# Kernel tuning notes

Measured on AMD Instinct MI355X. Metric: run time of the kernel, lower is better.

The kernel has to match this reference:

```python
import jax, jax.numpy as jnp
import numpy as np

B, C, N = 2, 64, 40000
MLP = [64, 64, 128]
EPS = 1e-5


def setup_inputs() -> dict:
    key = jax.random.key(0)
    ks = jax.random.split(key, 2 + 4 * len(MLP))
    inp = {
        "points": jax.random.normal(ks[0], (B, C, N), dtype=jnp.float32),
        "near_idx": jax.random.randint(ks[1], (N, 6), 0, 2 * N, dtype=jnp.int32),
    }
    last = 2 * C
    for i, out_ch in enumerate(MLP):
        k = 2 + 4 * i
        scale = 1.0 / np.sqrt(last)
        inp[f"W{i}"] = jax.random.normal(ks[k], (out_ch, last), dtype=jnp.float32) * scale
        inp[f"b{i}"] = jax.random.normal(ks[k + 1], (out_ch,), dtype=jnp.float32) * 0.01
        inp[f"g{i}"] = jnp.ones((out_ch,), dtype=jnp.float32)
        inp[f"beta{i}"] = jnp.zeros((out_ch,), dtype=jnp.float32)
        last = out_ch
    return inp


def _mlp_bn_relu(x, W, b, g, beta):
    # x: [B, N, 6, Cin]; 1x1 conv == channel matmul
    y = jnp.einsum("bnkc,oc->bnko", x, W) + b
    mu = y.mean(axis=(0, 1, 2))
    var = y.var(axis=(0, 1, 2))  # biased, matches BN training normalization
    y = (y - mu) * jax.lax.rsqrt(var + EPS) * g + beta
    return jax.nn.relu(y)


def reference(points, near_idx, W0, b0, g0, beta0, W1, b1, g1, beta1, W2, b2, g2, beta2):
    x = jnp.transpose(points, (0, 2, 1))          # [B, N, C]
    pad = jnp.full_like(x, -1.0)                  # out-of-index block (-1 fill)
    xpad = jnp.concatenate([x, pad], axis=1)      # [B, 2N, C]
    near = xpad[:, near_idx, :]                   # [B, N, 6, C] irregular gather
    feat = jnp.concatenate(
        [jnp.broadcast_to(x[:, :, None, :], near.shape), near], axis=3
    )                                             # [B, N, 6, 2C]
    feat = _mlp_bn_relu(feat, W0, b0, g0, beta0)
    feat = _mlp_bn_relu(feat, W1, b1, g1, beta1)
    feat = _mlp_bn_relu(feat, W2, b2, g2, beta2)  # [B, N, 6, C']
    new_feature = feat.max(axis=2)                # max over 6 neighbors -> [B, N, C']
    new_feature = jnp.transpose(new_feature, (0, 2, 1))  # [B, C', N] (torch layout)
    out_feature = new_feature.max(axis=1)         # max over channels -> [B, N]
    return (out_feature, new_feature)
```

## Files before the change

kernel.cpp:

```cpp
#include <hip/hip_runtime.h>

typedef unsigned short u16;
typedef unsigned int uint;
typedef short bf16x8 __attribute__((ext_vector_type(8)));
typedef float f32x4 __attribute__((ext_vector_type(4)));

constexpr int B_ = 2;
constexpr int N_ = 40000;
constexpr int SPB = 240000;
constexpr int S_ = B_ * SPB;
constexpr float EPS_ = 1e-5f;
constexpr float INV_S = 1.0f / (float)S_;
constexpr int OF_ = B_ * N_;

constexpr int WS_V_U16    = B_ * N_ * 128;
constexpr int WS_STATS_F  = WS_V_U16 / 2;
constexpr int WS_NEG2_F   = WS_STATS_F + 512;
constexpr int WS_PACK_U16 = WS_V_U16 + 2 * (512 + 64);
constexpr int MP_OFF  = 0;
constexpr int W1P_OFF = 8192;
constexpr int W2P_OFF = 12288;

__device__ inline float b2f_lo(uint u) { return __builtin_bit_cast(float, u << 16); }
__device__ inline float b2f_hi(uint u) { return __builtin_bit_cast(float, u & 0xffff0000u); }
__device__ inline float b2fu(u16 s)    { return __builtin_bit_cast(float, ((uint)s) << 16); }
__device__ inline u16 f2b(float f) {
    uint b = __builtin_bit_cast(uint, f);
    return (u16)((b + 0x7fffu + ((b >> 16) & 1u)) >> 16);
}
__device__ inline void unp8(uint4 q, float* f) {
    f[0] = b2f_lo(q.x); f[1] = b2f_hi(q.x); f[2] = b2f_lo(q.y); f[3] = b2f_hi(q.y);
    f[4] = b2f_lo(q.z); f[5] = b2f_hi(q.z); f[6] = b2f_lo(q.w); f[7] = b2f_hi(q.w);
}
__device__ inline uint fmap(float f) {
    int i = __float_as_int(f);
    return (i >= 0) ? ((uint)i | 0x80000000u) : ~(uint)i;
}
__device__ inline float funmap(uint u) {
    int i = (u & 0x80000000u) ? (int)(u & 0x7fffffffu) : (int)~u;
    return __int_as_float(i);
}

__global__ __launch_bounds__(256) void wprep_kernel(const float* __restrict__ W0,
                                                    const float* __restrict__ W1,
                                                    const float* __restrict__ W2,
                                                    float* __restrict__ stats,
                                                    float* __restrict__ neg2,
                                                    u16* __restrict__ pack) {
    const int t = threadIdx.x;
    stats[t] = 0.f; stats[t + 256] = 0.f;
    if (t < 64) {
        float s = 0.f;
        for (int j = 0; j < 64; ++j) s += W0[t * 128 + 64 + j];
        neg2[t] = -s;
    }
    for (int g = t; g < 40 * 64; g += 256) {
        int lane = g & 63, grp = g >> 6;
        int cb = lane & 15, kq = lane >> 4;
        ushort4 lo, hi;
        u16* dst;
        if (grp < 16) {
            int ct = grp >> 1, kk = grp & 1;
            int c = ct * 16 + cb, jb = kk * 32 + kq * 8;
            dst = pack + MP_OFF + g * 8;
            float v[8];
            #pragma unroll
            for (int i = 0; i < 8; ++i)
                v[i] = (c < 64) ? W0[c * 128 + jb + i] : W0[(c - 64) * 128 + 64 + jb + i];
            lo = {f2b(v[0]), f2b(v[1]), f2b(v[2]), f2b(v[3])};
            hi = {f2b(v[4]), f2b(v[5]), f2b(v[6]), f2b(v[7])};
        } else if (grp < 24) {
            int g2 = grp - 16;
            int ct = g2 >> 1, kk = g2 & 1;
            const float* wp = W1 + (ct * 16 + cb) * 64 + kk * 32 + kq * 8;
            dst = pack + W1P_OFF + (g2 * 64 + lane) * 8;
            lo = {f2b(wp[0]), f2b(wp[1]), f2b(wp[2]), f2b(wp[3])};
            hi = {f2b(wp[4]), f2b(wp[5]), f2b(wp[6]), f2b(wp[7])};
        } else {
            int g3 = grp - 24;
            int ct = g3 >> 1, kk = g3 & 1;
            const float* wp = W2 + (ct * 16 + cb) * 64 + kk * 32 + kq * 8;
            dst = pack + W2P_OFF + (g3 * 64 + lane) * 8;
            lo = {f2b(wp[0]), f2b(wp[1]), f2b(wp[2]), f2b(wp[3])};
            hi = {f2b(wp[4]), f2b(wp[5]), f2b(wp[6]), f2b(wp[7])};
        }
        *(ushort4*)dst = lo;
        *(ushort4*)(dst + 4) = hi;
    }
}

__global__ __launch_bounds__(256) void p0_kernel(const float* __restrict__ pts,
                                                 const u16* __restrict__ pack,
                                                 u16* __restrict__ V) {
    const int t = threadIdx.x, lane = t & 63, w = t >> 6;
    const int cb = lane & 15, kq = lane >> 4;
    const int b = blockIdx.y;
    const int n0 = blockIdx.x * 192 + w * 48;
    const uint4* mp = (const uint4*)(pack + MP_OFF);

    bf16x8 af[3][2];
    #pragma unroll
    for (int mt = 0; mt < 3; ++mt) {
        int n = n0 + mt * 16 + cb;
        int nc = (n < N_) ? n : (N_ - 1);
        const float* xp = pts + b * 64 * N_ + nc;
        #pragma unroll
        for (int kk = 0; kk < 2; ++kk) {
            int jb = kk * 32 + kq * 8;
            #pragma unroll
            for (int i = 0; i < 8; ++i)
                af[mt][kk][i] = (short)f2b(xp[(size_t)(jb + i) * N_]);
        }
    }
    #pragma unroll
    for (int ct = 0; ct < 8; ++ct) {
        bf16x8 b0 = __builtin_bit_cast(bf16x8, mp[(ct * 2 + 0) * 64 + lane]);
        bf16x8 b1 = __builtin_bit_cast(bf16x8, mp[(ct * 2 + 1) * 64 + lane]);
        #pragma unroll
        for (int mt = 0; mt < 3; ++mt) {
            f32x4 acc = {};
            acc = __builtin_amdgcn_mfma_f32_16x16x32_bf16(af[mt][0], b0, acc, 0, 0, 0);
            acc = __builtin_amdgcn_mfma_f32_16x16x32_bf16(af[mt][1], b1, acc, 0, 0, 0);
            int rbase = n0 + mt * 16 + kq * 4;
            #pragma unroll
            for (int r = 0; r < 4; ++r) {
                int n = rbase + r;
                if (n < N_) V[(size_t)(b * N_ + n) * 128 + ct * 16 + cb] = f2b(acc[r]);
            }
        }
    }
}

__global__ __launch_bounds__(256) void p1_kernel(const u16* __restrict__ V,
                                                 const int* __restrict__ nidx,
                                                 const float* __restrict__ neg2,
                                                 float* __restrict__ stats) {
    const int t = threadIdx.x;
    const int c = t & 63, sg = t >> 6;
    const int b = blockIdx.y;
    const int n0 = blockIdx.x * 32;
    const float ng = neg2[c];
    float sum = 0.f, sq = 0.f;
    for (int i = 0; i < 8; ++i) {
        int n = n0 + sg * 8 + i;
        float v1 = b2fu(V[(size_t)(b * N_ + n) * 128 + c]);
        #pragma unroll
        for (int k = 0; k < 6; ++k) {
            int m = nidx[n * 6 + k];
            float v2 = (m < N_) ? b2fu(V[(size_t)(b * N_ + m) * 128 + 64 + c]) : ng;
            float z = v1 + v2;
            sum += z; sq += z * z;
        }
    }
    __shared__ float red[2][4][64];
    red[0][sg][c] = sum;
    red[1][sg][c] = sq;
    __syncthreads();
    if (t < 64) {
        float s0 = (red[0][0][t] + red[0][1][t]) + (red[0][2][t] + red[0][3][t]);
        float q0 = (red[1][0][t] + red[1][1][t]) + (red[1][2][t] + red[1][3][t]);
        atomicAdd(&stats[t], s0);
        atomicAdd(&stats[64 + t], q0);
    }
}

__device__ inline bf16x8 build_af(const u16* __restrict__ V, int row1, int row2,
                                  const float* adt0, const float* adt1,
                                  const float* ngs, int j0) {
    float v1f[8], v2f[8];
    uint4 q1 = *(const uint4*)(V + (size_t)row1 * 128 + j0);
    unp8(q1, v1f);
    if (row2 >= 0) {
        uint4 q2 = *(const uint4*)(V + (size_t)row2 * 128 + 64 + j0);
        unp8(q2, v2f);
    } else {
        #pragma unroll
        for (int i = 0; i < 8; ++i) v2f[i] = ngs[j0 + i];
    }
    bf16x8 r;
    #pragma unroll
    for (int i = 0; i < 8; ++i) {
        float f0 = fmaxf((v1f[i] + v2f[i]) * adt0[j0 + i] + adt1[j0 + i], 0.f);
        r[i] = (short)f2b(f0);
    }
    return r;
}

__global__ __launch_bounds__(256) void p2_kernel(const u16* __restrict__ V,
                                                 const int* __restrict__ nidx,
                                                 const float* __restrict__ neg2,
                                                 const u16* __restrict__ pack,
                                                 const float* __restrict__ g0,
                                                 const float* __restrict__ beta0,
                                                 float* __restrict__ stats) {
    __shared__ float adt0[64], adt1[64], ngs[64];
    __shared__ float red[2][4][64];
    const int t = threadIdx.x, lane = t & 63, w = t >> 6;
    const int cb = lane & 15, kq = lane >> 4;
    if (t < 64) {
        float mu = stats[t] * INV_S, vr = stats[64 + t] * INV_S - mu * mu;
        float a = rsqrtf(vr + EPS_) * g0[t];
        adt0[t] = a; adt1[t] = beta0[t] - mu * a; ngs[t] = neg2[t];
    }
    __syncthreads();
    const int b = blockIdx.y;
    const int slb = blockIdx.x * 192 + w * 48;
    const uint4* w1p = (const uint4*)(pack + W1P_OFF);

    bf16x8 bf[4][2];
    #pragma unroll
    for (int ct = 0; ct < 4; ++ct)
        #pragma unroll
        for (int kk = 0; kk < 2; ++kk)
            bf[ct][kk] = __builtin_bit_cast(bf16x8, w1p[(ct * 2 + kk) * 64 + lane]);

    f32x4 acc[3][4] = {};
    #pragma unroll
    for (int mt = 0; mt < 3; ++mt) {
        int sl = slb + mt * 16 + cb;
        int n = sl / 6;
        int m = nidx[sl];
        int row1 = b * N_ + n;
        int row2 = (m < N_) ? (b * N_ + m) : -1;
        bf16x8 af[2];
        #pragma unroll
        for (int kk = 0; kk < 2; ++kk)
            af[kk] = build_af(V, row1, row2, adt0, adt1, ngs, kk * 32 + kq * 8);
        #pragma unroll
        for (int ct = 0; ct < 4; ++ct) {
            acc[mt][ct] = __builtin_amdgcn_mfma_f32_16x16x32_bf16(af[0], bf[ct][0], acc[mt][ct], 0, 0, 0);
            acc[mt][ct] = __builtin_amdgcn_mfma_f32_16x16x32_bf16(af[1], bf[ct][1], acc[mt][ct], 0, 0, 0);
        }
    }
    float ssum[4] = {0,0,0,0}, ssq[4] = {0,0,0,0};
    #pragma unroll
    for (int mt = 0; mt < 3; ++mt)
        #pragma unroll
        for (int ct = 0; ct < 4; ++ct)
            #pragma unroll
            for (int r = 0; r < 4; ++r) {
                float z = acc[mt][ct][r];
                ssum[ct] += z; ssq[ct] += z * z;
            }
    #pragma unroll
    for (int ct = 0; ct < 4; ++ct) {
        ssum[ct] += __shfl_xor(ssum[ct], 16); ssum[ct] += __shfl_xor(ssum[ct], 32);
        ssq[ct]  += __shfl_xor(ssq[ct], 16);  ssq[ct]  += __shfl_xor(ssq[ct], 32);
    }
    if (lane < 16) {
        #pragma unroll
        for (int ct = 0; ct < 4; ++ct) {
            red[0][w][ct * 16 + lane] = ssum[ct];
            red[1][w][ct * 16 + lane] = ssq[ct];
        }
    }
    __syncthreads();
    if (t < 64) {
        float s = (red[0][0][t] + red[0][1][t]) + (red[0][2][t] + red[0][3][t]);
        float q = (red[1][0][t] + red[1][1][t]) + (red[1][2][t] + red[1][3][t]);
        atomicAdd(&stats[128 + t], s);
        atomicAdd(&stats[192 + t], q);
    }
}

__global__ __launch_bounds__(256) void p3_kernel(const u16* __restrict__ V,
                                                 const int* __restrict__ nidx,
                                                 const float* __restrict__ neg2,
                                                 const u16* __restrict__ pack,
                                                 const float* __restrict__ g0, const float* __restrict__ beta0,
                                                 const float* __restrict__ g1, const float* __restrict__ beta1,
                                                 const float* __restrict__ g2,
                                                 float* __restrict__ stats,
                                                 float* __restrict__ out) {
    __shared__ u16  f1s[4][3072];
    __shared__ uint bmax[32][128];
    __shared__ float adt0[64], adt1[64], adt2[64], adt3[64], ngs[64];
    __shared__ float psign[128];
    __shared__ float red[2][4][128];
    const int t = threadIdx.x, lane = t & 63, w = t >> 6;
    const int cb = lane & 15, kq = lane >> 4;
    if (t < 64) {
        float mu0 = stats[t] * INV_S, vr0 = stats[64 + t] * INV_S - mu0 * mu0;
        float a0 = rsqrtf(vr0 + EPS_) * g0[t];
        adt0[t] = a0; adt1[t] = beta0[t] - mu0 * a0;
        float mu1 = stats[128 + t] * INV_S, vr1 = stats[192 + t] * INV_S - mu1 * mu1;
        float a1 = rsqrtf(vr1 + EPS_) * g1[t];
        adt2[t] = a1; adt3[t] = beta1[t] - mu1 * a1;
        ngs[t] = neg2[t];
    }
    if (t < 128) psign[t] = (g2[t] >= 0.f) ? 1.f : -1.f;
    #pragma unroll
    for (int i = 0; i < 16; ++i) ((uint*)bmax)[t + 256 * i] = 0u;
    __syncthreads();

    const int b = blockIdx.y;
    const int slb = blockIdx.x * 192 + w * 48;
    const uint4* w1p = (const uint4*)(pack + W1P_OFF);
    const uint4* w2p = (const uint4*)(pack + W2P_OFF);

    bf16x8 bf1[4][2];
    #pragma unroll
    for (int ct = 0; ct < 4; ++ct)
        #pragma unroll
        for (int kk = 0; kk < 2; ++kk)
            bf1[ct][kk] = __builtin_bit_cast(bf16x8, w1p[(ct * 2 + kk) * 64 + lane]);
    f32x4 acc1[3][4] = {};
    #pragma unroll
    for (int mt = 0; mt < 3; ++mt) {
        int sl = slb + mt * 16 + cb;
        int n = sl / 6;
        int m = nidx[sl];
        int row1 = b * N_ + n;
        int row2 = (m < N_) ? (b * N_ + m) : -1;
        bf16x8 af[2];
        #pragma unroll
        for (int kk = 0; kk < 2; ++kk)
            af[kk] = build_af(V, row1, row2, adt0, adt1, ngs, kk * 32 + kq * 8);
        #pragma unroll
        for (int ct = 0; ct < 4; ++ct) {
            acc1[mt][ct] = __builtin_amdgcn_mfma_f32_16x16x32_bf16(af[0], bf1[ct][0], acc1[mt][ct], 0, 0, 0);
            acc1[mt][ct] = __builtin_amdgcn_mfma_f32_16x16x32_bf16(af[1], bf1[ct][1], acc1[mt][ct], 0, 0, 0);
        }
    }
    u16* fb = f1s[w];
    #pragma unroll
    for (int mt = 0; mt < 3; ++mt)
        #pragma unroll
        for (int ct = 0; ct < 4; ++ct) {
            float a1c = adt2[ct * 16 + cb], d1c = adt3[ct * 16 + cb];
            #pragma unroll
            for (int r = 0; r < 4; ++r) {
                float f1 = fmaxf(acc1[mt][ct][r] * a1c + d1c, 0.f);
                int rl = mt * 16 + kq * 4 + r;
                fb[rl * 64 + ((ct * 16 + cb) ^ ((rl & 7) << 3))] = f2b(f1);
            }
        }
    float ssum[8] = {0,0,0,0,0,0,0,0}, ssq[8] = {0,0,0,0,0,0,0,0};
    #pragma unroll
    for (int half = 0; half < 2; ++half) {
        bf16x8 bf2[4][2];
        #pragma unroll
        for (int ct = 0; ct < 4; ++ct)
            #pragma unroll
            for (int kk = 0; kk < 2; ++kk)
                bf2[ct][kk] = __builtin_bit_cast(bf16x8, w2p[((half * 4 + ct) * 2 + kk) * 64 + lane]);
        f32x4 acc2[3][4] = {};
        #pragma unroll
        for (int mt = 0; mt < 3; ++mt) {
            int rl = mt * 16 + cb;
            bf16x8 af2[2];
            #pragma unroll
            for (int kk = 0; kk < 2; ++kk) {
                int j0 = kk * 32 + kq * 8;
                uint4 q = *(const uint4*)(fb + rl * 64 + (j0 ^ ((rl & 7) << 3)));
                af2[kk] = __builtin_bit_cast(bf16x8, q);
            }
            #pragma unroll
            for (int ct = 0; ct < 4; ++ct) {
                acc2[mt][ct] = __builtin_amdgcn_mfma_f32_16x16x32_bf16(af2[0], bf2[ct][0], acc2[mt][ct], 0, 0, 0);
                acc2[mt][ct] = __builtin_amdgcn_mfma_f32_16x16x32_bf16(af2[1], bf2[ct][1], acc2[mt][ct], 0, 0, 0);
            }
        }
        #pragma unroll
        for (int ct = 0; ct < 4; ++ct) {
            int c2 = half * 64 + ct * 16 + cb;
            float ps = psign[c2];
            #pragma unroll
            for (int mt = 0; mt < 3; ++mt) {
                int base = mt * 16 + kq * 4;
                int nb = 6 - (base % 6); nb = (nb > 4) ? 4 : nb;
                int nl = w * 8 + base / 6;
                float m1 = -3.402823466e+38f, m2 = -3.402823466e+38f;
                #pragma unroll
                for (int r = 0; r < 4; ++r) {
                    float z = acc2[mt][ct][r];
                    ssum[half * 4 + ct] += z;
                    ssq[half * 4 + ct] += z * z;
                    float zz = z * ps;
                    m1 = (r < nb) ? fmaxf(m1, zz) : m1;
                    m2 = (r < nb) ? m2 : fmaxf(m2, zz);
                }
                atomicMax(&bmax[nl][c2], fmap(m1));
                if (nb < 4) atomicMax(&bmax[nl + 1][c2], fmap(m2));
            }
        }
    }
    #pragma unroll
    for (int j = 0; j < 8; ++j) {
        ssum[j] += __shfl_xor(ssum[j], 16); ssum[j] += __shfl_xor(ssum[j], 32);
        ssq[j]  += __shfl_xor(ssq[j], 16);  ssq[j]  += __shfl_xor(ssq[j], 32);
    }
    if (lane < 16) {
        #pragma unroll
        for (int j = 0; j < 8; ++j) {
            int c = (j >> 2) * 64 + (j & 3) * 16 + lane;
            red[0][w][c] = ssum[j];
            red[1][w][c] = ssq[j];
        }
    }
    __syncthreads();
    if (t < 128) {
        float s = (red[0][0][t] + red[0][1][t]) + (red[0][2][t] + red[0][3][t]);
        float q = (red[1][0][t] + red[1][1][t]) + (red[1][2][t] + red[1][3][t]);
        atomicAdd(&stats[256 + t], s);
        atomicAdd(&stats[384 + t], q);
    }
    {
        int c2 = t >> 1, nh = t & 1;
        float ps = psign[c2];
        float* op = out + OF_ + ((size_t)b * 128 + c2) * N_ + blockIdx.x * 32 + nh * 16;
        #pragma unroll
        for (int i4 = 0; i4 < 4; ++i4) {
            float4 v;
            v.x = funmap(bmax[nh * 16 + i4 * 4 + 0][c2]) * ps;
            v.y = funmap(bmax[nh * 16 + i4 * 4 + 1][c2]) * ps;
            v.z = funmap(bmax[nh * 16 + i4 * 4 + 2][c2]) * ps;
            v.w = funmap(bmax[nh * 16 + i4 * 4 + 3][c2]) * ps;
            *(float4*)(op + i4 * 4) = v;
        }
    }
}

__global__ __launch_bounds__(256) void p4_kernel(const float* __restrict__ g2,
                                                 const float* __restrict__ beta2,
                                                 const float* __restrict__ stats,
                                                 float* __restrict__ outbuf) {
    __shared__ float a2s[128], d2s[128];
    const int t = threadIdx.x;
    if (t < 128) {
        float mu = stats[256 + t] * INV_S;
        float vr = stats[384 + t] * INV_S - mu * mu;
        float a = rsqrtf(vr + EPS_) * g2[t];
        a2s[t] = a;
        d2s[t] = beta2[t] - mu * a;
    }
    __syncthreads();
    const int b = blockIdx.y;
    const int n = blockIdx.x * 256 + t;
    if (n >= N_) return;
    float vmax = -3.402823466e+38f;
    #pragma unroll 8
    for (int c2 = 0; c2 < 128; ++c2) {
        size_t idx = OF_ + ((size_t)b * 128 + c2) * N_ + n;
        float v = fmaxf(outbuf[idx] * a2s[c2] + d2s[c2], 0.f);
        outbuf[idx] = v;
        vmax = fmaxf(vmax, v);
    }
    outbuf[b * N_ + n] = vmax;
}

extern "C" void kernel_launch(void* const* d_in, const int* in_sizes, int n_in,
                              void* d_out, int out_size, void* d_ws, size_t ws_size,
                              hipStream_t stream) {
    (void)in_sizes; (void)n_in; (void)out_size; (void)ws_size;
    const float* pts   = (const float*)d_in[0];
    const int*   nidx  = (const int*)d_in[1];
    const float* W0    = (const float*)d_in[2];
    const float* g0    = (const float*)d_in[4];
    const float* beta0 = (const float*)d_in[5];
    const float* W1    = (const float*)d_in[6];
    const float* g1    = (const float*)d_in[8];
    const float* beta1 = (const float*)d_in[9];
    const float* W2    = (const float*)d_in[10];
    const float* g2    = (const float*)d_in[12];
    const float* beta2 = (const float*)d_in[13];
    u16*   V     = (u16*)d_ws;
    float* stats = (float*)d_ws + WS_STATS_F;
    float* neg2  = (float*)d_ws + WS_NEG2_F;
    u16*   pack  = (u16*)d_ws + WS_PACK_U16;
    float* out   = (float*)d_out;

    hipLaunchKernelGGL(wprep_kernel, dim3(1), dim3(256), 0, stream, W0, W1, W2, stats, neg2, pack);
    hipLaunchKernelGGL(p0_kernel, dim3((N_ + 191) / 192, B_), dim3(256), 0, stream, pts, pack, V);
    hipLaunchKernelGGL(p1_kernel, dim3(N_ / 32, B_), dim3(256), 0, stream, V, nidx, neg2, stats);
    hipLaunchKernelGGL(p2_kernel, dim3(SPB / 192, B_), dim3(256), 0, stream, V, nidx, neg2, pack, g0, beta0, stats);
    hipLaunchKernelGGL(p3_kernel, dim3(SPB / 192, B_), dim3(256), 0, stream, V, nidx, neg2, pack,
                       g0, beta0, g1, beta1, g2, stats, out);
    hipLaunchKernelGGL(p4_kernel, dim3((N_ + 255) / 256, B_), dim3(256), 0, stream, g2, beta2, stats, out);
}
```

Baseline: 367.8 us.

## Cache layer-0 activations in workspace and vectorize p1 stats gather

```diff
diff --git a/kernel.cpp b/kernel.cpp
--- a/kernel.cpp
+++ b/kernel.cpp
@@ -12,18 +12,13 @@
 constexpr float EPS_ = 1e-5f;
 constexpr float INV_S = 1.0f / (float)S_;
 constexpr int OF_ = B_ * N_;
-
-constexpr int WS_V_U16    = B_ * N_ * 128;
-constexpr int WS_STATS_F  = WS_V_U16 / 2;
-constexpr int WS_NEG2_F   = WS_STATS_F + 512;
-constexpr int WS_PACK_U16 = WS_V_U16 + 2 * (512 + 64);
-constexpr int MP_OFF  = 0;
-constexpr int W1P_OFF = 8192;
-constexpr int W2P_OFF = 12288;
+constexpr int TILES_PB = SPB / 48;
+
+constexpr int      WS_V_U16   = B_ * N_ * 128;
+constexpr size_t   NEED_BIG_B = 81955072ull;
 
 __device__ inline float b2f_lo(uint u) { return __builtin_bit_cast(float, u << 16); }
 __device__ inline float b2f_hi(uint u) { return __builtin_bit_cast(float, u & 0xffff0000u); }
-__device__ inline float b2fu(u16 s)    { return __builtin_bit_cast(float, ((uint)s) << 16); }
 __device__ inline u16 f2b(float f) {
     uint b = __builtin_bit_cast(uint, f);
     return (u16)((b + 0x7fffu + ((b >> 16) & 1u)) >> 16);
@@ -62,7 +57,7 @@
         if (grp < 16) {
             int ct = grp >> 1, kk = grp & 1;
             int c = ct * 16 + cb, jb = kk * 32 + kq * 8;
-            dst = pack + MP_OFF + g * 8;
+            dst = pack + g * 8;
             float v[8];
             #pragma unroll
             for (int i = 0; i < 8; ++i)
@@ -73,14 +68,14 @@
             int g2 = grp - 16;
             int ct = g2 >> 1, kk = g2 & 1;
             const float* wp = W1 + (ct * 16 + cb) * 64 + kk * 32 + kq * 8;
-            dst = pack + W1P_OFF + (g2 * 64 + lane) * 8;
+            dst = pack + 8192 + (g2 * 64 + lane) * 8;
             lo = {f2b(wp[0]), f2b(wp[1]), f2b(wp[2]), f2b(wp[3])};
             hi = {f2b(wp[4]), f2b(wp[5]), f2b(wp[6]), f2b(wp[7])};
         } else {
             int g3 = grp - 24;
             int ct = g3 >> 1, kk = g3 & 1;
             const float* wp = W2 + (ct * 16 + cb) * 64 + kk * 32 + kq * 8;
-            dst = pack + W2P_OFF + (g3 * 64 + lane) * 8;
+            dst = pack + 12288 + (g3 * 64 + lane) * 8;
             lo = {f2b(wp[0]), f2b(wp[1]), f2b(wp[2]), f2b(wp[3])};
             hi = {f2b(wp[4]), f2b(wp[5]), f2b(wp[6]), f2b(wp[7])};
         }
@@ -96,7 +91,7 @@
     const int cb = lane & 15, kq = lane >> 4;
     const int b = blockIdx.y;
     const int n0 = blockIdx.x * 192 + w * 48;
-    const uint4* mp = (const uint4*)(pack + MP_OFF);
+    const uint4* mp = (const uint4*)pack;
 
     bf16x8 af[3][2];
     #pragma unroll
@@ -135,32 +130,47 @@
                                                  const int* __restrict__ nidx,
                                                  const float* __restrict__ neg2,
                                                  float* __restrict__ stats) {
-    const int t = threadIdx.x;
-    const int c = t & 63, sg = t >> 6;
+    const int t = threadIdx.x, lane = t & 63, w = t >> 6;
+    const int slot = lane >> 3, cg = lane & 7;
     const int b = blockIdx.y;
-    const int n0 = blockIdx.x * 32;
-    const float ng = neg2[c];
-    float sum = 0.f, sq = 0.f;
+    const int s0 = blockIdx.x * 384 + w * 96;
+    float ngs8[8];
+    #pragma unroll
+    for (int i = 0; i < 8; ++i) ngs8[i] = neg2[cg * 8 + i];
+    float sum[8] = {0,0,0,0,0,0,0,0}, sq[8] = {0,0,0,0,0,0,0,0};
+    #pragma unroll 4
+    for (int it = 0; it < 12; ++it) {
+        int s = s0 + it * 8 + slot;
+        int n = s / 6;
+        int m = nidx[s];
+        bool valid = (m < N_);
+        int row2 = valid ? (b * N_ + m) : 0;
+        uint4 q1 = *(const uint4*)(V + (size_t)(b * N_ + n) * 128 + cg * 8);
+        uint4 q2 = *(const uint4*)(V + (size_t)row2 * 128 + 64 + cg * 8);
+        float v1[8], v2[8];
+        unp8(q1, v1); unp8(q2, v2);
+        #pragma unroll
+        for (int i = 0; i < 8; ++i) {
+            float z = v1[i] + (valid ? v2[i] : ngs8[i]);
+            sum[i] += z; sq[i] = fmaf(z, z, sq[i]);
+        }
+    }
+    #pragma unroll
     for (int i = 0; i < 8; ++i) {
-        int n = n0 + sg * 8 + i;
-        float v1 = b2fu(V[(size_t)(b * N_ + n) * 128 + c]);
-        #pragma unroll
-        for (int k = 0; k < 6; ++k) {
-            int m = nidx[n * 6 + k];
-            float v2 = (m < N_) ? b2fu(V[(size_t)(b * N_ + m) * 128 + 64 + c]) : ng;
-            float z = v1 + v2;
-            sum += z; sq += z * z;
-        }
+        sum[i] += __shfl_xor(sum[i], 8); sum[i] += __shfl_xor(sum[i], 16); sum[i] += __shfl_xor(sum[i], 32);
+        sq[i]  += __shfl_xor(sq[i], 8);  sq[i]  += __shfl_xor(sq[i], 16);  sq[i]  += __shfl_xor(sq[i], 32);
     }
     __shared__ float red[2][4][64];
-    red[0][sg][c] = sum;
-    red[1][sg][c] = sq;
+    if (slot == 0) {
+        #pragma unroll
+        for (int i = 0; i < 8; ++i) { red[0][w][cg * 8 + i] = sum[i]; red[1][w][cg * 8 + i] = sq[i]; }
+    }
     __syncthreads();
     if (t < 64) {
-        float s0 = (red[0][0][t] + red[0][1][t]) + (red[0][2][t] + red[0][3][t]);
-        float q0 = (red[1][0][t] + red[1][1][t]) + (red[1][2][t] + red[1][3][t]);
-        atomicAdd(&stats[t], s0);
-        atomicAdd(&stats[64 + t], q0);
+        float s_ = (red[0][0][t] + red[0][1][t]) + (red[0][2][t] + red[0][3][t]);
+        float q_ = (red[1][0][t] + red[1][1][t]) + (red[1][2][t] + red[1][3][t]);
+        atomicAdd(&stats[t], s_);
+        atomicAdd(&stats[64 + t], q_);
     }
 }
 
@@ -186,13 +196,15 @@
     return r;
 }
 
+template<int STOREF0>
 __global__ __launch_bounds__(256) void p2_kernel(const u16* __restrict__ V,
                                                  const int* __restrict__ nidx,
                                                  const float* __restrict__ neg2,
                                                  const u16* __restrict__ pack,
                                                  const float* __restrict__ g0,
                                                  const float* __restrict__ beta0,
-                                                 float* __restrict__ stats) {
+                                                 float* __restrict__ stats,
+                                                 u16* __restrict__ f0buf) {
     __shared__ float adt0[64], adt1[64], ngs[64];
     __shared__ float red[2][4][64];
     const int t = threadIdx.x, lane = t & 63, w = t >> 6;
@@ -205,7 +217,8 @@
     __syncthreads();
     const int b = blockIdx.y;
     const int slb = blockIdx.x * 192 + w * 48;
-    const uint4* w1p = (const uint4*)(pack + W1P_OFF);
+    const uint4* w1p = (const uint4*)(pack + 8192);
+    uint4* ftile = STOREF0 ? ((uint4*)f0buf + ((size_t)b * TILES_PB + blockIdx.x * 4 + w) * (6 * 64)) : nullptr;
 
     bf16x8 bf[4][2];
     #pragma unroll
@@ -224,8 +237,11 @@
         int row2 = (m < N_) ? (b * N_ + m) : -1;
         bf16x8 af[2];
         #pragma unroll
-        for (int kk = 0; kk < 2; ++kk)
+        for (int kk = 0; kk < 2; ++kk) {
             af[kk] = build_af(V, row1, row2, adt0, adt1, ngs, kk * 32 + kq * 8);
+            if constexpr (STOREF0)
+                ftile[(mt * 2 + kk) * 64 + lane] = __builtin_bit_cast(uint4, af[kk]);
+        }
         #pragma unroll
         for (int ct = 0; ct < 4; ++ct) {
             acc[mt][ct] = __builtin_amdgcn_mfma_f32_16x16x32_bf16(af[0], bf[ct][0], acc[mt][ct], 0, 0, 0);
@@ -263,6 +279,7 @@
     }
 }
 
+template<int LOADF0>
 __global__ __launch_bounds__(256) void p3_kernel(const u16* __restrict__ V,
                                                  const int* __restrict__ nidx,
                                                  const float* __restrict__ neg2,
@@ -271,6 +288,7 @@
                                                  const float* __restrict__ g1, const float* __restrict__ beta1,
                                                  const float* __restrict__ g2,
                                                  float* __restrict__ stats,
+                                                 const u16* __restrict__ f0buf,
                                                  float* __restrict__ out) {
     __shared__ u16  f1s[4][3072];
     __shared__ uint bmax[32][128];
@@ -280,13 +298,15 @@
     const int t = threadIdx.x, lane = t & 63, w = t >> 6;
     const int cb = lane & 15, kq = lane >> 4;
     if (t < 64) {
-        float mu0 = stats[t] * INV_S, vr0 = stats[64 + t] * INV_S - mu0 * mu0;
-        float a0 = rsqrtf(vr0 + EPS_) * g0[t];
-        adt0[t] = a0; adt1[t] = beta0[t] - mu0 * a0;
+        if constexpr (!LOADF0) {
+            float mu0 = stats[t] * INV_S, vr0 = stats[64 + t] * INV_S - mu0 * mu0;
+            float a0 = rsqrtf(vr0 + EPS_) * g0[t];
+            adt0[t] = a0; adt1[t] = beta0[t] - mu0 * a0;
+            ngs[t] = neg2[t];
+        }
         float mu1 = stats[128 + t] * INV_S, vr1 = stats[192 + t] * INV_S - mu1 * mu1;
         float a1 = rsqrtf(vr1 + EPS_) * g1[t];
         adt2[t] = a1; adt3[t] = beta1[t] - mu1 * a1;
-        ngs[t] = neg2[t];
     }
     if (t < 128) psign[t] = (g2[t] >= 0.f) ? 1.f : -1.f;
     #pragma unroll
@@ -295,8 +315,9 @@
 
     const int b = blockIdx.y;
     const int slb = blockIdx.x * 192 + w * 48;
-    const uint4* w1p = (const uint4*)(pack + W1P_OFF);
-    const uint4* w2p = (const uint4*)(pack + W2P_OFF);
+    const uint4* w1p = (const uint4*)(pack + 8192);
+    const uint4* w2p = (const uint4*)(pack + 12288);
+    const uint4* ftile = LOADF0 ? ((const uint4*)f0buf + ((size_t)b * TILES_PB + blockIdx.x * 4 + w) * (6 * 64)) : nullptr;
 
     bf16x8 bf1[4][2];
     #pragma unroll
@@ -307,15 +328,20 @@
     f32x4 acc1[3][4] = {};
     #pragma unroll
     for (int mt = 0; mt < 3; ++mt) {
-        int sl = slb + mt * 16 + cb;
-        int n = sl / 6;
-        int m = nidx[sl];
-        int row1 = b * N_ + n;
-        int row2 = (m < N_) ? (b * N_ + m) : -1;
         bf16x8 af[2];
-        #pragma unroll
-        for (int kk = 0; kk < 2; ++kk)
-            af[kk] = build_af(V, row1, row2, adt0, adt1, ngs, kk * 32 + kq * 8);
+        if constexpr (LOADF0) {
+            af[0] = __builtin_bit_cast(bf16x8, ftile[(mt * 2 + 0) * 64 + lane]);
+            af[1] = __builtin_bit_cast(bf16x8, ftile[(mt * 2 + 1) * 64 + lane]);
+        } else {
+            int sl = slb + mt * 16 + cb;
+            int n = sl / 6;
+            int m = nidx[sl];
+            int row1 = b * N_ + n;
+            int row2 = (m < N_) ? (b * N_ + m) : -1;
+            #pragma unroll
+            for (int kk = 0; kk < 2; ++kk)
+                af[kk] = build_af(V, row1, row2, adt0, adt1, ngs, kk * 32 + kq * 8);
+        }
         #pragma unroll
         for (int ct = 0; ct < 4; ++ct) {
             acc1[mt][ct] = __builtin_amdgcn_mfma_f32_16x16x32_bf16(af[0], bf1[ct][0], acc1[mt][ct], 0, 0, 0);
@@ -452,7 +478,7 @@
 extern "C" void kernel_launch(void* const* d_in, const int* in_sizes, int n_in,
                               void* d_out, int out_size, void* d_ws, size_t ws_size,
                               hipStream_t stream) {
-    (void)in_sizes; (void)n_in; (void)out_size; (void)ws_size;
+    (void)in_sizes; (void)n_in; (void)out_size;
     const float* pts   = (const float*)d_in[0];
     const int*   nidx  = (const int*)d_in[1];
     const float* W0    = (const float*)d_in[2];
@@ -464,17 +490,27 @@
     const float* W2    = (const float*)d_in[10];
     const float* g2    = (const float*)d_in[12];
     const float* beta2 = (const float*)d_in[13];
+    const bool big = ws_size >= NEED_BIG_B;
     u16*   V     = (u16*)d_ws;
-    float* stats = (float*)d_ws + WS_STATS_F;
-    float* neg2  = (float*)d_ws + WS_NEG2_F;
-    u16*   pack  = (u16*)d_ws + WS_PACK_U16;
+    u16*   f0b   = big ? ((u16*)d_ws + WS_V_U16) : nullptr;
+    float* stats = (float*)d_ws + (big ? 20480000 : 5120000);
+    float* neg2  = stats + 512;
+    u16*   pack  = (u16*)d_ws + (big ? 40961152 : 10241152);
     float* out   = (float*)d_out;
 
     hipLaunchKernelGGL(wprep_kernel, dim3(1), dim3(256), 0, stream, W0, W1, W2, stats, neg2, pack);
     hipLaunchKernelGGL(p0_kernel, dim3((N_ + 191) / 192, B_), dim3(256), 0, stream, pts, pack, V);
-    hipLaunchKernelGGL(p1_kernel, dim3(N_ / 32, B_), dim3(256), 0, stream, V, nidx, neg2, stats);
-    hipLaunchKernelGGL(p2_kernel, dim3(SPB / 192, B_), dim3(256), 0, stream, V, nidx, neg2, pack, g0, beta0, stats);
-    hipLaunchKernelGGL(p3_kernel, dim3(SPB / 192, B_), dim3(256), 0, stream, V, nidx, neg2, pack,
-                       g0, beta0, g1, beta1, g2, stats, out);
+    hipLaunchKernelGGL(p1_kernel, dim3(SPB / 384, B_), dim3(256), 0, stream, V, nidx, neg2, stats);
+    if (big) {
+        hipLaunchKernelGGL((p2_kernel<1>), dim3(SPB / 192, B_), dim3(256), 0, stream,
+                           V, nidx, neg2, pack, g0, beta0, stats, f0b);
+        hipLaunchKernelGGL((p3_kernel<1>), dim3(SPB / 192, B_), dim3(256), 0, stream,
+                           V, nidx, neg2, pack, g0, beta0, g1, beta1, g2, stats, f0b, out);
+    } else {
+        hipLaunchKernelGGL((p2_kernel<0>), dim3(SPB / 192, B_), dim3(256), 0, stream,
+                           V, nidx, neg2, pack, g0, beta0, stats, f0b);
+        hipLaunchKernelGGL((p3_kernel<0>), dim3(SPB / 192, B_), dim3(256), 0, stream,
+                           V, nidx, neg2, pack, g0, beta0, g1, beta1, g2, stats, f0b, out);
+    }
     hipLaunchKernelGGL(p4_kernel, dim3((N_ + 255) / 256, B_), dim3(256), 0, stream, g2, beta2, stats, out);
 }
```

Result: faster. 313.2 us (-14.9%).
